# Optimization experiments

Hardware: AMD Instinct MI355X
Metric: run time of the kernel (lower is better)

The kernel has to match this reference:

```python
import jax, jax.numpy as jnp
import numpy as np

WORD_DIM = 200
ASPECT_DIM = 32
NUM_NEG = 2
AVG_RATING = 3.8
LR_RATING = 1.0
LR_ABAE = 1.0


def setup_inputs() -> dict:
    key = jax.random.key(0)
    ks = jax.random.split(key, 20)
    R, L, D, A, B, NNZ = 20000, 30, WORD_DIM, ASPECT_DIM, 4096, 65536
    e_w = jax.random.normal(ks[0], (R, L, D), jnp.float32)
    y_s = jax.random.normal(ks[1], (R, D), jnp.float32)
    z_n = jax.random.normal(ks[2], (R * NUM_NEG, D), jnp.float32)
    label = jax.random.uniform(ks[3], (B,), jnp.float32, 1.0, 5.0)
    u_idx = jnp.stack([jax.random.randint(ks[4], (NNZ,), 0, B),
                       jax.random.randint(ks[5], (NNZ,), 0, R)]).astype(jnp.int64)
    i_idx = jnp.stack([jax.random.randint(ks[6], (NNZ,), 0, B),
                       jax.random.randint(ks[7], (NNZ,), 0, R)]).astype(jnp.int64)
    u_val = jax.random.uniform(ks[8], (NNZ,), jnp.float32)
    i_val = jax.random.uniform(ks[9], (NNZ,), jnp.float32)
    s = 0.05
    M_w = jax.random.normal(ks[10], (D, D), jnp.float32) * s
    M_b = jnp.zeros((D,), jnp.float32)
    W_w = jax.random.normal(ks[11], (A, D), jnp.float32) * s
    W_b = jnp.zeros((A,), jnp.float32)
    T_w = jax.random.normal(ks[12], (D, A), jnp.float32) * s
    T_b = jnp.zeros((D,), jnp.float32)
    fc_w = jax.random.uniform(ks[13], (1, A), jnp.float32, -0.05, 0.05)
    fc_b = jnp.zeros((1,), jnp.float32)
    fm_V = jax.random.uniform(ks[14], (A, 10), jnp.float32, -0.05, 0.05)
    return dict(e_w=e_w, y_s=y_s, z_n=z_n, label=label,
                user_histor_value=u_val, item_histor_value=i_val,
                M_w=M_w, M_b=M_b, W_w=W_w, W_b=W_b, T_w=T_w, T_b=T_b,
                fc_w=fc_w, fc_b=fc_b, fm_V=fm_V,
                user_histor_index=u_idx, item_histor_index=i_idx)


def _l2norm(x, axis):
    return x / jnp.maximum(jnp.linalg.norm(x, axis=axis, keepdims=True), 1e-12)


def reference(e_w, y_s, z_n, label, user_histor_value, item_histor_value,
              M_w, M_b, W_w, W_b, T_w, T_b, fc_w, fc_b, fm_V,
              user_histor_index, item_histor_index):
    R, L, D = e_w.shape
    A = W_w.shape[0]
    B = label.shape[0]
    # ABAE attention: dx = (e_w @ M^T + b) . y_s  -> (R, L)
    Me = jnp.einsum('rld,ed->rle', e_w, M_w) + M_b  # (R, L, D)
    dx = jnp.einsum('rld,rd->rl', Me, y_s)
    ax = jax.nn.softmax(dx, axis=1)                 # attention over words
    z_s = jnp.einsum('rld,rl->rd', e_w, ax)         # (R, D) weighted sentence emb
    p_t = z_s @ W_w.T + W_b                         # (R, A) aspect weights
    r_s = p_t @ T_w.T + T_b                         # (R, D) reconstructed emb
    # margin ranking (hinge) loss on cosine similarities
    c1 = jnp.sum(_l2norm(r_s, 1) * _l2norm(z_s, 1), axis=-1, keepdims=True)  # (R,1)
    c1 = jnp.tile(c1, (1, NUM_NEG)).reshape(-1)                              # (R*neg,)
    zn = _l2norm(z_n.reshape(R, NUM_NEG, D), 2)
    c2 = jnp.sum(zn * _l2norm(r_s, 1)[:, None, :], axis=-1).reshape(-1)
    abae_out_loss = jnp.maximum(0.0, 1.0 - (c1 - c2))
    J_loss = jnp.mean(abae_out_loss)
    # orthogonality regularizer on aspect matrix columns
    Tn = _l2norm(T_w, 0)                            # normalize each column (dim=0)
    G = Tn.T @ Tn                                   # (A, A)
    U_loss = jnp.mean((G - jnp.eye(A, dtype=G.dtype)) ** 2)
    abae_loss = U_loss + J_loss
    # sparse pooling: (B, R) sparse @ (R, A)
    u_rows, u_cols = user_histor_index[0], user_histor_index[1]
    i_rows, i_cols = item_histor_index[0], item_histor_index[1]
    user_aspect = jax.ops.segment_sum(p_t[u_cols] * user_histor_value[:, None],
                                      u_rows, num_segments=B)
    item_aspect = jax.ops.segment_sum(p_t[i_cols] * item_histor_value[:, None],
                                      i_rows, num_segments=B)
    output_emb = user_aspect * item_aspect          # (B, A)
    # factorization machine
    fm_linear = output_emb @ fc_w.T + fc_b          # (B, 1)
    i1 = (output_emb @ fm_V) ** 2
    i2 = (output_emb ** 2) @ (fm_V ** 2)
    # NOTE: faithful to source -- the 0.5*sum reduces over ALL elements (scalar)
    fm_output = 0.5 * jnp.sum(i1 - i2) + fm_linear  # (B, 1)
    prediction = fm_output + jnp.float32(AVG_RATING)
    rating_out_loss = (prediction.reshape(-1) - label) ** 2
    rating_loss = jnp.mean(rating_out_loss)
    obj = LR_RATING * rating_loss + LR_ABAE * abae_loss
    return (obj, rating_out_loss, abae_out_loss, prediction, user_aspect, item_aspect)
```

## Files before the change

kernel.cpp:

```cpp
#include <hip/hip_runtime.h>
#include <hip/hip_bf16.h>
#include <math.h>

#define R_CNT   20000
#define L_CNT   30
#define D_CNT   200
#define A_CNT   32
#define B_CNT   4096
#define NNZ_CNT 65536
#define AVG_RATING 3.8f

#define NW 1536
#define TAIL_GRID 5000

#define OUT_OBJ  0
#define OUT_RL   1
#define OUT_AB   (1 + B_CNT)
#define OUT_PRED (OUT_AB + 2*R_CNT)
#define OUT_UA   (OUT_PRED + B_CNT)
#define OUT_IA   (OUT_UA + B_CNT*A_CNT)

#define WS_DBL    0
#define WS_MODE   32
#define WS_FMLIN  64
#define WS_PT     16448
#define WS_V      2576448
#define WS_JPART  18627648
#define WS_SPART  18667648
#define WS_UPART  18671744

#define WAITV16() do { asm volatile("s_waitcnt vmcnt(16)" ::: "memory"); \
                       __builtin_amdgcn_sched_barrier(0); } while (0)
#define SB0() __builtin_amdgcn_sched_barrier(0)

__device__ __forceinline__ float4 blk_reduce4(float4 v, float4* scratch) {
    __syncthreads();
    #pragma unroll
    for (int o = 32; o >= 1; o >>= 1) {
        v.x += __shfl_xor(v.x, o);
        v.y += __shfl_xor(v.y, o);
        v.z += __shfl_xor(v.z, o);
        v.w += __shfl_xor(v.w, o);
    }
    int w = threadIdx.x >> 6;
    if ((threadIdx.x & 63) == 0) scratch[w] = v;
    __syncthreads();
    float4 t0 = scratch[0], t1 = scratch[1], t2 = scratch[2], t3 = scratch[3];
    return make_float4(t0.x + t1.x + t2.x + t3.x,
                       t0.y + t1.y + t2.y + t3.y,
                       t0.z + t1.z + t2.z + t3.z,
                       t0.w + t1.w + t2.w + t3.w);
}

__global__ __launch_bounds__(256) void k_pre(const float* __restrict__ y_s,
                                             const float* __restrict__ M_w,
                                             const float* __restrict__ T_w,
                                             const int* __restrict__ u_idx,
                                             float* __restrict__ V,
                                             float* __restrict__ upart,
                                             float* __restrict__ out,
                                             double* __restrict__ dbl,
                                             int* __restrict__ mode) {
    __shared__ __align__(16) float sh[8224];
    const int tid = threadIdx.x;
    const int bid = blockIdx.x;

    if (bid < 313) {
        float* Msh = sh;
        float* Ysh = sh + 6500;
        int r0 = bid * 64;
        int dg = tid & 31, rg = tid >> 5;
        float acc[8][8];
        #pragma unroll
        for (int i = 0; i < 8; i++)
            #pragma unroll
            for (int j = 0; j < 8; j++) acc[i][j] = 0.f;
        for (int e0 = 0; e0 < D_CNT; e0 += 25) {
            __syncthreads();
            for (int idx = tid; idx < 25 * 256; idx += 256) {
                int ee = idx >> 8, d = idx & 255;
                Msh[ee * 260 + d] = (d < D_CNT) ? M_w[(e0 + ee) * D_CNT + d] : 0.f;
            }
            for (int idx = tid; idx < 25 * 64; idx += 256) {
                int rr = idx / 25, ee = idx - rr * 25;
                int row = r0 + rr;
                Ysh[ee * 68 + rr] = (row < R_CNT) ? y_s[row * D_CNT + e0 + ee] : 0.f;
            }
            __syncthreads();
            for (int ee = 0; ee < 25; ee++) {
                const float4 ya = *(const float4*)&Ysh[ee * 68 + rg * 8];
                const float4 yb = *(const float4*)&Ysh[ee * 68 + rg * 8 + 4];
                const float4 ma = *(const float4*)&Msh[ee * 260 + dg * 8];
                const float4 mb = *(const float4*)&Msh[ee * 260 + dg * 8 + 4];
                float ys[8] = {ya.x, ya.y, ya.z, ya.w, yb.x, yb.y, yb.z, yb.w};
                float ms[8] = {ma.x, ma.y, ma.z, ma.w, mb.x, mb.y, mb.z, mb.w};
                #pragma unroll
                for (int i = 0; i < 8; i++)
                    #pragma unroll
                    for (int j = 0; j < 8; j++)
                        acc[i][j] = fmaf(ys[i], ms[j], acc[i][j]);
            }
        }
        if (dg < 25) {
            #pragma unroll
            for (int i = 0; i < 8; i++) {
                int row = r0 + rg * 8 + i;
                if (row < R_CNT) {
                    *(float4*)&V[row * D_CNT + dg * 8]     = make_float4(acc[i][0], acc[i][1], acc[i][2], acc[i][3]);
                    *(float4*)&V[row * D_CNT + dg * 8 + 4] = make_float4(acc[i][4], acc[i][5], acc[i][6], acc[i][7]);
                }
            }
        }
    } else if (bid < 345) {
        float* Tsh = sh;
        float* tn  = sh + 6400;
        float4* red4 = (float4*)(sh + 6448);
        for (int idx = tid; idx < 1600; idx += 256)
            ((float4*)Tsh)[idx] = ((const float4*)T_w)[idx];
        __syncthreads();
        int a = tid >> 3, k = tid & 7;
        float p = 0.f;
        #pragma unroll
        for (int j = 0; j < 25; ++j) { float t = Tsh[(k + 8*j)*32 + a]; p = fmaf(t, t, p); }
        p += __shfl_xor(p, 1); p += __shfl_xor(p, 2); p += __shfl_xor(p, 4);
        if (k == 0) tn[a] = fmaxf(sqrtf(p), 1e-12f);
        __syncthreads();
        const int i = bid - 313;
        float s = 0.f;
        #pragma unroll
        for (int j = 0; j < 25; ++j)
            s = fmaf(Tsh[(k + 8*j)*32 + i], Tsh[(k + 8*j)*32 + a], s);
        s += __shfl_xor(s, 1); s += __shfl_xor(s, 2); s += __shfl_xor(s, 4);
        float part = 0.f;
        if (k == 0) {
            float g = s / (tn[i] * tn[a]);
            float diff = g - ((i == a) ? 1.f : 0.f);
            part = diff * diff;
        }
        float4 tot = blk_reduce4(make_float4(part, 0.f, 0.f, 0.f), red4);
        if (tid == 0) upart[i] = tot.x;
    } else {
        int base = (bid - 345) * 2048;
        #pragma unroll
        for (int j = 0; j < 8; ++j)
            out[OUT_UA + base + j * 256 + tid] = 0.f;
        if (bid == 345 && tid == 0) {
            dbl[0] = 0.0; dbl[1] = 0.0; dbl[2] = 0.0;
            int m = 1;
            for (int i = 1; i < 256; i += 2) if (u_idx[i] != 0) { m = 0; break; }
            *mode = m;
        }
    }
}

__device__ __forceinline__ void stage_chunk(const float* src, float* lds,
                                            int lane, const float* ew_last4) {
    #pragma unroll
    for (int i = 0; i < 12; ++i) {
        const float* p = src + i * 256 + lane * 4;
        if (p > ew_last4) p = ew_last4;
        __builtin_amdgcn_global_load_lds(
            (const __attribute__((address_space(1))) unsigned int*)p,
            (__attribute__((address_space(3))) unsigned int*)(lds + i * 256),
            16, 0, 0);
    }
}
__device__ __forceinline__ void stage_v(const float* vsrc, float* lds, int lane) {
    #pragma unroll
    for (int i = 0; i < 4; ++i)
        __builtin_amdgcn_global_load_lds(
            (const __attribute__((address_space(1))) unsigned int*)(vsrc + i * 64 + lane),
            (__attribute__((address_space(3))) unsigned int*)(lds + i * 64),
            4, 0, 0);
}

__device__ __forceinline__ void chunk_pass(const float* __restrict__ eb,
                                           const float* __restrict__ vb,
                                           float* __restrict__ dxs,
                                           int lane, float& m, float& s,
                                           float4& zacc) {
    int l = lane >> 2, k = lane & 3;
    float p = 0.f;
    if (l < 15) {
        const float4* er = (const float4*)(eb + l * 200);
        const float4* vr = (const float4*)vb;
        #pragma unroll
        for (int t = 0; t < 13; ++t) {
            int idx = k + 4 * t;
            if (idx < 50) {
                float4 e = er[idx], v = vr[idx];
                p += e.x * v.x + e.y * v.y + e.z * v.z + e.w * v.w;
            }
        }
    }
    p += __shfl_xor(p, 1);
    p += __shfl_xor(p, 2);
    if (l < 15 && k == 0) dxs[l] = p;
    float4 d0 = ((const float4*)dxs)[0];
    float4 d1 = ((const float4*)dxs)[1];
    float4 d2 = ((const float4*)dxs)[2];
    float4 d3 = ((const float4*)dxs)[3];
    float dx[15] = {d0.x, d0.y, d0.z, d0.w, d1.x, d1.y, d1.z, d1.w,
                    d2.x, d2.y, d2.z, d2.w, d3.x, d3.y, d3.z};
    float cm = dx[0];
    #pragma unroll
    for (int q = 1; q < 15; ++q) cm = fmaxf(cm, dx[q]);
    float mn = fmaxf(m, cm);
    float sc = __expf(m - mn);
    float w[15];
    float ss = 0.f;
    #pragma unroll
    for (int q = 0; q < 15; ++q) { w[q] = __expf(dx[q] - mn); ss += w[q]; }
    s = s * sc + ss;
    zacc.x *= sc; zacc.y *= sc; zacc.z *= sc; zacc.w *= sc;
    if (lane < 50) {
        #pragma unroll
        for (int q = 0; q < 15; ++q) {
            float4 e = ((const float4*)(eb + q * 200))[lane];
            zacc.x = fmaf(w[q], e.x, zacc.x);
            zacc.y = fmaf(w[q], e.y, zacc.y);
            zacc.z = fmaf(w[q], e.z, zacc.z);
            zacc.w = fmaf(w[q], e.w, zacc.w);
        }
    }
    m = mn;
}

__global__ __launch_bounds__(64) void k_zs(const float* __restrict__ e_w,
                                           float* __restrict__ V) {
    __shared__ __align__(16) float bufE[2][3072];
    __shared__ __align__(16) float bufV[2][256];
    const int lane = threadIdx.x;
    const float* ew_last4 = e_w + (size_t)R_CNT * 6000 - 4;

    int rev = blockIdx.x;
    stage_v(V + (size_t)rev * 200, bufV[0], lane);
    stage_chunk(e_w + (size_t)rev * 6000, bufE[0], lane, ew_last4);
    int pv = 0;
    for (;;) {
        float m = -3.0e38f, s = 0.f;
        float4 zacc = make_float4(0.f, 0.f, 0.f, 0.f);
        SB0();
        stage_chunk(e_w + (size_t)rev * 6000 + 3000, bufE[1], lane, ew_last4);
        int rnext = rev + NW;
        bool last = (rnext >= R_CNT);
        int rc = last ? rev : rnext;
        stage_v(V + (size_t)rc * 200, bufV[pv ^ 1], lane);
        WAITV16();
        chunk_pass(bufE[0], bufV[pv], bufV[pv] + 208, lane, m, s, zacc);
        SB0();
        stage_chunk(e_w + (size_t)rc * 6000, bufE[0], lane, ew_last4);
        WAITV16();
        chunk_pass(bufE[1], bufV[pv], bufV[pv] + 208, lane, m, s, zacc);
        float inv = 1.f / s;
        if (lane < 50) {
            float4 z = make_float4(zacc.x * inv, zacc.y * inv,
                                   zacc.z * inv, zacc.w * inv);
            ((float4*)(V + (size_t)rev * 200))[lane] = z;
        }
        if (last) break;
        rev = rnext;
        pv ^= 1;
    }
}

__global__ __launch_bounds__(256) void k_tail(const float* __restrict__ zs,
                                              const float* __restrict__ z_n,
                                              const float* __restrict__ W_w,
                                              const float* __restrict__ W_b,
                                              const float* __restrict__ T_w,
                                              const float* __restrict__ T_b,
                                              float* __restrict__ p_t,
                                              float* __restrict__ out,
                                              double* __restrict__ jpart) {
    __shared__ __align__(16) float zsh[4 * D_CNT];
    __shared__ float pts[4 * 32];
    __shared__ float4 red[8];
    const int tid = threadIdx.x;
    const int w = tid >> 6;
    const int r0 = blockIdx.x * 4;

    for (int i = tid; i < 200; i += 256)
        ((float4*)zsh)[i] = ((const float4*)(zs + (size_t)r0 * D_CNT))[i];

    float zn[8];
    #pragma unroll
    for (int q = 0; q < 8; ++q) zn[q] = 0.f;
    if (tid < D_CNT) {
        #pragma unroll
        for (int q = 0; q < 4; ++q) {
            zn[2*q]   = z_n[(size_t)(2*(r0+q))     * D_CNT + tid];
            zn[2*q+1] = z_n[(size_t)(2*(r0+q) + 1) * D_CNT + tid];
        }
    }
    __syncthreads();

    {
        int a = tid >> 3, k = tid & 7;
        float a0 = 0.f, a1 = 0.f, a2 = 0.f, a3 = 0.f;
        #pragma unroll
        for (int j = 0; j < 25; ++j) {
            float wv = W_w[a * D_CNT + k + 8 * j];
            a0 = fmaf(zsh[0*D_CNT + k + 8*j], wv, a0);
            a1 = fmaf(zsh[1*D_CNT + k + 8*j], wv, a1);
            a2 = fmaf(zsh[2*D_CNT + k + 8*j], wv, a2);
            a3 = fmaf(zsh[3*D_CNT + k + 8*j], wv, a3);
        }
        #pragma unroll
        for (int o = 1; o < 8; o <<= 1) {
            a0 += __shfl_xor(a0, o); a1 += __shfl_xor(a1, o);
            a2 += __shfl_xor(a2, o); a3 += __shfl_xor(a3, o);
        }
        if (k == 0) {
            float wbv = W_b[a];
            float p0 = a0 + wbv, p1 = a1 + wbv, p2 = a2 + wbv, p3 = a3 + wbv;
            pts[0*32+a] = p0; pts[1*32+a] = p1; pts[2*32+a] = p2; pts[3*32+a] = p3;
            p_t[(size_t)(r0+0) * 32 + a] = p0;
            p_t[(size_t)(r0+1) * 32 + a] = p1;
            p_t[(size_t)(r0+2) * 32 + a] = p2;
            p_t[(size_t)(r0+3) * 32 + a] = p3;
        }
    }
    __syncthreads();

    float rv[4] = {0.f, 0.f, 0.f, 0.f};
    float zv[4] = {0.f, 0.f, 0.f, 0.f};
    if (tid < D_CNT) {
        float tbv = T_b[tid];
        rv[0] = tbv; rv[1] = tbv; rv[2] = tbv; rv[3] = tbv;
        const float4* tw = (const float4*)(T_w + tid * 32);
        #pragma unroll
        for (int u = 0; u < 8; ++u) {
            float4 t = tw[u];
            #pragma unroll
            for (int q = 0; q < 4; ++q) {
                rv[q] = fmaf(t.x, pts[q*32 + 4*u + 0], rv[q]);
                rv[q] = fmaf(t.y, pts[q*32 + 4*u + 1], rv[q]);
                rv[q] = fmaf(t.z, pts[q*32 + 4*u + 2], rv[q]);
                rv[q] = fmaf(t.w, pts[q*32 + 4*u + 3], rv[q]);
            }
        }
        #pragma unroll
        for (int q = 0; q < 4; ++q) zv[q] = zsh[q * D_CNT + tid];
    }

    double jloc = 0.0;
    #pragma unroll
    for (int q = 0; q < 4; ++q) {
        float4 Av = make_float4(rv[q]*rv[q], rv[q]*zv[q], zv[q]*zv[q], zn[2*q]*zn[2*q]);
        float4 Bv = make_float4(zn[2*q]*rv[q], zn[2*q+1]*zn[2*q+1], zn[2*q+1]*rv[q], 0.f);
        #pragma unroll
        for (int o = 32; o >= 1; o >>= 1) {
            Av.x += __shfl_xor(Av.x, o); Av.y += __shfl_xor(Av.y, o);
            Av.z += __shfl_xor(Av.z, o); Av.w += __shfl_xor(Av.w, o);
            Bv.x += __shfl_xor(Bv.x, o); Bv.y += __shfl_xor(Bv.y, o);
            Bv.z += __shfl_xor(Bv.z, o);
        }
        if ((tid & 63) == 0) { red[2*w] = Av; red[2*w+1] = Bv; }
        __syncthreads();
        if (tid == 0) {
            float rr = 0.f, rz = 0.f, zz = 0.f, n00 = 0.f, n0r = 0.f, n11 = 0.f, n1r = 0.f;
            #pragma unroll
            for (int i = 0; i < 4; ++i) {
                float4 a = red[2*i], b = red[2*i+1];
                rr += a.x; rz += a.y; zz += a.z; n00 += a.w;
                n0r += b.x; n11 += b.y; n1r += b.z;
            }
            float nr = fmaxf(sqrtf(rr), 1e-12f);
            float nz = fmaxf(sqrtf(zz), 1e-12f);
            float c1  = rz  / (nr * nz);
            float c20 = n0r / (fmaxf(sqrtf(n00), 1e-12f) * nr);
            float c21 = n1r / (fmaxf(sqrtf(n11), 1e-12f) * nr);
            float l0 = fmaxf(0.f, 1.f - (c1 - c20));
            float l1 = fmaxf(0.f, 1.f - (c1 - c21));
            out[OUT_AB + 2 * (r0 + q)]     = l0;
            out[OUT_AB + 2 * (r0 + q) + 1] = l1;
            jloc += (double)l0 + (double)l1;
        }
        __syncthreads();
    }
    if (tid == 0) jpart[blockIdx.x] = jloc;
}

__global__ __launch_bounds__(256) void k_scatter(const int* __restrict__ u_idx,
                                                 const int* __restrict__ i_idx,
                                                 const float* __restrict__ u_val,
                                                 const float* __restrict__ i_val,
                                                 const float* __restrict__ p_t,
                                                 const int* __restrict__ mode,
                                                 float* __restrict__ out) {
    long long gid = (long long)blockIdx.x * 256 + threadIdx.x;
    const long long HALF = (long long)NNZ_CNT * 32;
    int is_item = gid >= HALF;
    long long rem = gid - (is_item ? HALF : 0);
    int k = (int)(rem >> 5), a = (int)(rem & 31);
    const int* idx = is_item ? i_idx : u_idx;
    const float* val = is_item ? i_val : u_val;
    int m64 = *mode;
    int row, col;
    if (m64) { row = idx[2 * k]; col = idx[2 * (NNZ_CNT + k)]; }
    else     { row = idx[k];     col = idx[NNZ_CNT + k]; }
    float v = p_t[col * 32 + a] * val[k];
    float* base = out + (is_item ? OUT_IA : OUT_UA);
    atomicAdd(&base[row * 32 + a], v);
}

__global__ __launch_bounds__(256) void k_fm(const float* __restrict__ out,
                                            const float* __restrict__ fc_w,
                                            const float* __restrict__ fc_b,
                                            const float* __restrict__ fm_V,
                                            float* __restrict__ fm_lin,
                                            double* __restrict__ spart) {
    __shared__ float parts[8];
    int tid = threadIdx.x;
    int a = tid & 31;
    int b = blockIdx.x * 8 + (tid >> 5);
    float ua = out[OUT_UA + b * 32 + a];
    float ia = out[OUT_IA + b * 32 + a];
    float oe = ua * ia;
    float oe2 = oe * oe;
    float lin = oe * fc_w[a];
    #pragma unroll
    for (int o = 1; o < 32; o <<= 1) lin += __shfl_xor(lin, o);
    float part = 0.f;
    #pragma unroll
    for (int j = 0; j < 10; j++) {
        float v = fm_V[a * 10 + j];
        float s1 = oe * v;
        float s2 = oe2 * v * v;
        #pragma unroll
        for (int o = 1; o < 32; o <<= 1) { s1 += __shfl_xor(s1, o); s2 += __shfl_xor(s2, o); }
        part += s1 * s1 - s2;
    }
    if (a == 0) {
        fm_lin[b] = lin + fc_b[0];
        parts[tid >> 5] = part;
    }
    __syncthreads();
    if (tid == 0) {
        float s = 0.f;
        #pragma unroll
        for (int i = 0; i < 8; ++i) s += parts[i];
        spart[blockIdx.x] = 0.5 * (double)s;
    }
}

__global__ __launch_bounds__(256) void k_predfinal(const float* __restrict__ label,
                                                   const float* __restrict__ fm_lin,
                                                   const double* __restrict__ spart,
                                                   const double* __restrict__ jpart,
                                                   const float* __restrict__ upart,
                                                   float* __restrict__ out) {
    __shared__ double dred[4];
    __shared__ float Ssh;
    __shared__ float ured[4];
    int tid = threadIdx.x;
    double sl = spart[tid] + spart[tid + 256];
    #pragma unroll
    for (int o = 32; o >= 1; o >>= 1) sl += __shfl_xor(sl, o);
    if ((tid & 63) == 0) dred[tid >> 6] = sl;
    __syncthreads();
    if (tid == 0) Ssh = (float)(dred[0] + dred[1] + dred[2] + dred[3]);
    __syncthreads();
    float S = Ssh;
    double racc = 0.0;
    #pragma unroll
    for (int i = 0; i < 16; ++i) {
        int b = tid + 256 * i;
        float pred = fm_lin[b] + S + AVG_RATING;
        float d = pred - label[b];
        float rl = d * d;
        out[OUT_PRED + b] = pred;
        out[OUT_RL + b] = rl;
        racc += (double)rl;
    }
    double jacc = 0.0;
    for (int i = tid; i < TAIL_GRID; i += 256) jacc += jpart[i];
    float u = (tid < 32) ? upart[tid] : 0.f;
    #pragma unroll
    for (int o = 32; o >= 1; o >>= 1) {
        racc += __shfl_xor(racc, o);
        jacc += __shfl_xor(jacc, o);
        u    += __shfl_xor(u, o);
    }
    __syncthreads();
    if ((tid & 63) == 0) dred[tid >> 6] = racc;
    __syncthreads();
    double rsum = dred[0] + dred[1] + dred[2] + dred[3];
    __syncthreads();
    if ((tid & 63) == 0) dred[tid >> 6] = jacc;
    __syncthreads();
    double jsum = dred[0] + dred[1] + dred[2] + dred[3];
    if ((tid & 63) == 0) ured[tid >> 6] = u;
    __syncthreads();
    if (tid == 0) {
        double U = (double)(ured[0] + ured[1] + ured[2] + ured[3]) / 1024.0;
        double J = jsum / (2.0 * R_CNT);
        double RL = rsum / (double)B_CNT;
        out[OUT_OBJ] = (float)(RL + U + J);
    }
}

extern "C" void kernel_launch(void* const* d_in, const int* in_sizes, int n_in,
                              void* d_out, int out_size, void* d_ws, size_t ws_size,
                              hipStream_t stream) {
    const float* e_w   = (const float*)d_in[0];
    const float* y_s   = (const float*)d_in[1];
    const float* z_n   = (const float*)d_in[2];
    const float* label = (const float*)d_in[3];
    const float* u_val = (const float*)d_in[4];
    const float* i_val = (const float*)d_in[5];
    const float* M_w   = (const float*)d_in[6];
    const float* W_w   = (const float*)d_in[8];
    const float* W_b   = (const float*)d_in[9];
    const float* T_w   = (const float*)d_in[10];
    const float* T_b   = (const float*)d_in[11];
    const float* fc_w  = (const float*)d_in[12];
    const float* fc_b  = (const float*)d_in[13];
    const float* fm_V  = (const float*)d_in[14];
    const int*   u_idx = (const int*)d_in[15];
    const int*   i_idx = (const int*)d_in[16];

    float* out = (float*)d_out;
    char* ws = (char*)d_ws;
    double* dbl   = (double*)(ws + WS_DBL);
    int* mode     = (int*)(ws + WS_MODE);
    float* fm_lin = (float*)(ws + WS_FMLIN);
    float* p_t    = (float*)(ws + WS_PT);
    float* V      = (float*)(ws + WS_V);
    double* jpart = (double*)(ws + WS_JPART);
    double* spart = (double*)(ws + WS_SPART);
    float* upart  = (float*)(ws + WS_UPART);

    k_pre<<<473, 256, 0, stream>>>(y_s, M_w, T_w, u_idx, V, upart, out, dbl, mode);
    k_zs<<<NW, 64, 0, stream>>>(e_w, V);
    k_tail<<<TAIL_GRID, 256, 0, stream>>>(V, z_n, W_w, W_b, T_w, T_b, p_t, out, jpart);
    k_scatter<<<(2 * NNZ_CNT * 32) / 256, 256, 0, stream>>>(u_idx, i_idx, u_val, i_val,
                                                            p_t, mode, out);
    k_fm<<<B_CNT / 8, 256, 0, stream>>>(out, fc_w, fc_b, fm_V, fm_lin, spart);
    k_predfinal<<<1, 256, 0, stream>>>(label, fm_lin, spart, jpart, upart, out);
}
```

Before: 323.5 us.

## Fuse tail projection and hinge-loss computation into the streaming z_s kernel

Measured after the change: 329.1 us. Within noise of the previous version (+1.7%).

```diff
diff --git a/kernel.cpp b/kernel.cpp
--- a/kernel.cpp
+++ b/kernel.cpp
@@ -11,7 +11,6 @@
 #define AVG_RATING 3.8f
 
 #define NW 1536
-#define TAIL_GRID 5000
 
 #define OUT_OBJ  0
 #define OUT_RL   1
@@ -29,8 +28,8 @@
 #define WS_SPART  18667648
 #define WS_UPART  18671744
 
-#define WAITV16() do { asm volatile("s_waitcnt vmcnt(16)" ::: "memory"); \
-                       __builtin_amdgcn_sched_barrier(0); } while (0)
+#define WAITV(N) do { asm volatile("s_waitcnt vmcnt(" #N ")" ::: "memory"); \
+                      __builtin_amdgcn_sched_barrier(0); } while (0)
 #define SB0() __builtin_amdgcn_sched_barrier(0)
 
 __device__ __forceinline__ float4 blk_reduce4(float4 v, float4* scratch) {
@@ -227,145 +226,121 @@
 }
 
 __global__ __launch_bounds__(64) void k_zs(const float* __restrict__ e_w,
-                                           float* __restrict__ V) {
+                                           const float* __restrict__ V,
+                                           const float* __restrict__ z_n,
+                                           const float* __restrict__ W_w,
+                                           const float* __restrict__ W_b,
+                                           const float* __restrict__ T_w,
+                                           const float* __restrict__ T_b,
+                                           float* __restrict__ p_t,
+                                           float* __restrict__ out,
+                                           double* __restrict__ jpart) {
     __shared__ __align__(16) float bufE[2][3072];
     __shared__ __align__(16) float bufV[2][256];
     const int lane = threadIdx.x;
+    const bool act = lane < 50;
+    const int dl = act ? lane : 0;
     const float* ew_last4 = e_w + (size_t)R_CNT * 6000 - 4;
 
+    const float wb = W_b[lane >> 1];
+    float4 tbv = make_float4(0.f, 0.f, 0.f, 0.f);
+    if (act) tbv = ((const float4*)T_b)[dl];
+    float tb[4] = {tbv.x, tbv.y, tbv.z, tbv.w};
+
+    double jloc = 0.0;
     int rev = blockIdx.x;
     stage_v(V + (size_t)rev * 200, bufV[0], lane);
     stage_chunk(e_w + (size_t)rev * 6000, bufE[0], lane, ew_last4);
     int pv = 0;
     for (;;) {
+        int rnext = rev + NW;
+        bool last = (rnext >= R_CNT);
+        int rc = last ? rev : rnext;
         float m = -3.0e38f, s = 0.f;
         float4 zacc = make_float4(0.f, 0.f, 0.f, 0.f);
         SB0();
         stage_chunk(e_w + (size_t)rev * 6000 + 3000, bufE[1], lane, ew_last4);
-        int rnext = rev + NW;
-        bool last = (rnext >= R_CNT);
-        int rc = last ? rev : rnext;
         stage_v(V + (size_t)rc * 200, bufV[pv ^ 1], lane);
-        WAITV16();
+        float4 zn0 = make_float4(0.f, 0.f, 0.f, 0.f);
+        float4 zn1 = make_float4(0.f, 0.f, 0.f, 0.f);
+        if (act) {
+            zn0 = ((const float4*)(z_n + (size_t)(2 * rev) * 200))[lane];
+            zn1 = ((const float4*)(z_n + (size_t)(2 * rev + 1) * 200))[lane];
+        }
+        WAITV(18);
         chunk_pass(bufE[0], bufV[pv], bufV[pv] + 208, lane, m, s, zacc);
         SB0();
         stage_chunk(e_w + (size_t)rc * 6000, bufE[0], lane, ew_last4);
-        WAITV16();
+        WAITV(18);
         chunk_pass(bufE[1], bufV[pv], bufV[pv] + 208, lane, m, s, zacc);
-        float inv = 1.f / s;
-        if (lane < 50) {
-            float4 z = make_float4(zacc.x * inv, zacc.y * inv,
-                                   zacc.z * inv, zacc.w * inv);
-            ((float4*)(V + (size_t)rev * 200))[lane] = z;
-        }
-        if (last) break;
-        rev = rnext;
-        pv ^= 1;
-    }
-}
-
-__global__ __launch_bounds__(256) void k_tail(const float* __restrict__ zs,
-                                              const float* __restrict__ z_n,
-                                              const float* __restrict__ W_w,
-                                              const float* __restrict__ W_b,
-                                              const float* __restrict__ T_w,
-                                              const float* __restrict__ T_b,
-                                              float* __restrict__ p_t,
-                                              float* __restrict__ out,
-                                              double* __restrict__ jpart) {
-    __shared__ __align__(16) float zsh[4 * D_CNT];
-    __shared__ float pts[4 * 32];
-    __shared__ float4 red[8];
-    const int tid = threadIdx.x;
-    const int w = tid >> 6;
-    const int r0 = blockIdx.x * 4;
-
-    for (int i = tid; i < 200; i += 256)
-        ((float4*)zsh)[i] = ((const float4*)(zs + (size_t)r0 * D_CNT))[i];
-
-    float zn[8];
-    #pragma unroll
-    for (int q = 0; q < 8; ++q) zn[q] = 0.f;
-    if (tid < D_CNT) {
-        #pragma unroll
-        for (int q = 0; q < 4; ++q) {
-            zn[2*q]   = z_n[(size_t)(2*(r0+q))     * D_CNT + tid];
-            zn[2*q+1] = z_n[(size_t)(2*(r0+q) + 1) * D_CNT + tid];
-        }
-    }
-    __syncthreads();
-
-    {
-        int a = tid >> 3, k = tid & 7;
-        float a0 = 0.f, a1 = 0.f, a2 = 0.f, a3 = 0.f;
-        #pragma unroll
-        for (int j = 0; j < 25; ++j) {
-            float wv = W_w[a * D_CNT + k + 8 * j];
-            a0 = fmaf(zsh[0*D_CNT + k + 8*j], wv, a0);
-            a1 = fmaf(zsh[1*D_CNT + k + 8*j], wv, a1);
-            a2 = fmaf(zsh[2*D_CNT + k + 8*j], wv, a2);
-            a3 = fmaf(zsh[3*D_CNT + k + 8*j], wv, a3);
-        }
-        #pragma unroll
-        for (int o = 1; o < 8; o <<= 1) {
-            a0 += __shfl_xor(a0, o); a1 += __shfl_xor(a1, o);
-            a2 += __shfl_xor(a2, o); a3 += __shfl_xor(a3, o);
-        }
-        if (k == 0) {
-            float wbv = W_b[a];
-            float p0 = a0 + wbv, p1 = a1 + wbv, p2 = a2 + wbv, p3 = a3 + wbv;
-            pts[0*32+a] = p0; pts[1*32+a] = p1; pts[2*32+a] = p2; pts[3*32+a] = p3;
-            p_t[(size_t)(r0+0) * 32 + a] = p0;
-            p_t[(size_t)(r0+1) * 32 + a] = p1;
-            p_t[(size_t)(r0+2) * 32 + a] = p2;
-            p_t[(size_t)(r0+3) * 32 + a] = p3;
-        }
-    }
-    __syncthreads();
-
-    float rv[4] = {0.f, 0.f, 0.f, 0.f};
-    float zv[4] = {0.f, 0.f, 0.f, 0.f};
-    if (tid < D_CNT) {
-        float tbv = T_b[tid];
-        rv[0] = tbv; rv[1] = tbv; rv[2] = tbv; rv[3] = tbv;
-        const float4* tw = (const float4*)(T_w + tid * 32);
-        #pragma unroll
-        for (int u = 0; u < 8; ++u) {
-            float4 t = tw[u];
+
+        float* zsh  = bufE[1];
+        float* ptsL = bufE[1] + 208;
+        const float inv = 1.f / s;
+        float zf[4] = {zacc.x * inv, zacc.y * inv, zacc.z * inv, zacc.w * inv};
+        if (act) ((float4*)zsh)[dl] = make_float4(zf[0], zf[1], zf[2], zf[3]);
+
+        {
+            int a = lane >> 1, half = lane & 1;
+            const float4* wrow = (const float4*)(W_w + a * 200);
+            const float4* zrow = (const float4*)zsh;
+            float p = 0.f;
             #pragma unroll
-            for (int q = 0; q < 4; ++q) {
-                rv[q] = fmaf(t.x, pts[q*32 + 4*u + 0], rv[q]);
-                rv[q] = fmaf(t.y, pts[q*32 + 4*u + 1], rv[q]);
-                rv[q] = fmaf(t.z, pts[q*32 + 4*u + 2], rv[q]);
-                rv[q] = fmaf(t.w, pts[q*32 + 4*u + 3], rv[q]);
-            }
-        }
-        #pragma unroll
-        for (int q = 0; q < 4; ++q) zv[q] = zsh[q * D_CNT + tid];
-    }
-
-    double jloc = 0.0;
-    #pragma unroll
-    for (int q = 0; q < 4; ++q) {
-        float4 Av = make_float4(rv[q]*rv[q], rv[q]*zv[q], zv[q]*zv[q], zn[2*q]*zn[2*q]);
-        float4 Bv = make_float4(zn[2*q]*rv[q], zn[2*q+1]*zn[2*q+1], zn[2*q+1]*rv[q], 0.f);
-        #pragma unroll
-        for (int o = 32; o >= 1; o >>= 1) {
-            Av.x += __shfl_xor(Av.x, o); Av.y += __shfl_xor(Av.y, o);
-            Av.z += __shfl_xor(Av.z, o); Av.w += __shfl_xor(Av.w, o);
-            Bv.x += __shfl_xor(Bv.x, o); Bv.y += __shfl_xor(Bv.y, o);
-            Bv.z += __shfl_xor(Bv.z, o);
-        }
-        if ((tid & 63) == 0) { red[2*w] = Av; red[2*w+1] = Bv; }
-        __syncthreads();
-        if (tid == 0) {
-            float rr = 0.f, rz = 0.f, zz = 0.f, n00 = 0.f, n0r = 0.f, n11 = 0.f, n1r = 0.f;
-            #pragma unroll
-            for (int i = 0; i < 4; ++i) {
-                float4 a = red[2*i], b = red[2*i+1];
-                rr += a.x; rz += a.y; zz += a.z; n00 += a.w;
-                n0r += b.x; n11 += b.y; n1r += b.z;
-            }
+            for (int t = 0; t < 25; ++t) {
+                int idx = half + 2 * t;
+                float4 wv = wrow[idx];
+                float4 zv = zrow[idx];
+                p += wv.x * zv.x + wv.y * zv.y + wv.z * zv.z + wv.w * zv.w;
+            }
+            p += __shfl_xor(p, 1);
+            float pt = p + wb;
+            if (half == 0) {
+                ptsL[a] = pt;
+                p_t[(size_t)rev * 32 + a] = pt;
+            }
+        }
+
+        float rr = 0.f, rz = 0.f, zz = 0.f, n00 = 0.f, n0r = 0.f, n11 = 0.f, n1r = 0.f;
+        {
+            const float4* pt4 = (const float4*)ptsL;
+            float4 pq0 = pt4[0], pq1 = pt4[1], pq2 = pt4[2], pq3 = pt4[3];
+            float4 pq4 = pt4[4], pq5 = pt4[5], pq6 = pt4[6], pq7 = pt4[7];
+            if (act) {
+                float znf0[4] = {zn0.x, zn0.y, zn0.z, zn0.w};
+                float znf1[4] = {zn1.x, zn1.y, zn1.z, zn1.w};
+                #pragma unroll
+                for (int j = 0; j < 4; ++j) {
+                    int d = 4 * dl + j;
+                    const float4* trow = (const float4*)(T_w + d * 32);
+                    float r = tb[j];
+                    float4 t0 = trow[0], t1 = trow[1], t2 = trow[2], t3 = trow[3];
+                    float4 t4 = trow[4], t5 = trow[5], t6 = trow[6], t7 = trow[7];
+                    r += t0.x*pq0.x + t0.y*pq0.y + t0.z*pq0.z + t0.w*pq0.w;
+                    r += t1.x*pq1.x + t1.y*pq1.y + t1.z*pq1.z + t1.w*pq1.w;
+                    r += t2.x*pq2.x + t2.y*pq2.y + t2.z*pq2.z + t2.w*pq2.w;
+                    r += t3.x*pq3.x + t3.y*pq3.y + t3.z*pq3.z + t3.w*pq3.w;
+                    r += t4.x*pq4.x + t4.y*pq4.y + t4.z*pq4.z + t4.w*pq4.w;
+                    r += t5.x*pq5.x + t5.y*pq5.y + t5.z*pq5.z + t5.w*pq5.w;
+                    r += t6.x*pq6.x + t6.y*pq6.y + t6.z*pq6.z + t6.w*pq6.w;
+                    r += t7.x*pq7.x + t7.y*pq7.y + t7.z*pq7.z + t7.w*pq7.w;
+                    rr  += r * r;
+                    rz  += r * zf[j];
+                    zz  += zf[j] * zf[j];
+                    n00 += znf0[j] * znf0[j];
+                    n0r += znf0[j] * r;
+                    n11 += znf1[j] * znf1[j];
+                    n1r += znf1[j] * r;
+                }
+            }
+        }
+        #pragma unroll
+        for (int o = 1; o < 64; o <<= 1) {
+            rr  += __shfl_xor(rr, o);  rz  += __shfl_xor(rz, o);
+            zz  += __shfl_xor(zz, o);  n00 += __shfl_xor(n00, o);
+            n0r += __shfl_xor(n0r, o); n11 += __shfl_xor(n11, o);
+            n1r += __shfl_xor(n1r, o);
+        }
+        if (lane == 0) {
             float nr = fmaxf(sqrtf(rr), 1e-12f);
             float nz = fmaxf(sqrtf(zz), 1e-12f);
             float c1  = rz  / (nr * nz);
@@ -373,13 +348,15 @@
             float c21 = n1r / (fmaxf(sqrtf(n11), 1e-12f) * nr);
             float l0 = fmaxf(0.f, 1.f - (c1 - c20));
             float l1 = fmaxf(0.f, 1.f - (c1 - c21));
-            out[OUT_AB + 2 * (r0 + q)]     = l0;
-            out[OUT_AB + 2 * (r0 + q) + 1] = l1;
+            out[OUT_AB + 2 * rev]     = l0;
+            out[OUT_AB + 2 * rev + 1] = l1;
             jloc += (double)l0 + (double)l1;
         }
-        __syncthreads();
-    }
-    if (tid == 0) jpart[blockIdx.x] = jloc;
+        if (last) break;
+        rev = rnext;
+        pv ^= 1;
+    }
+    if (lane == 0) jpart[blockIdx.x] = jloc;
 }
 
 __global__ __launch_bounds__(256) void k_scatter(const int* __restrict__ u_idx,
@@ -475,7 +452,7 @@
         racc += (double)rl;
     }
     double jacc = 0.0;
-    for (int i = tid; i < TAIL_GRID; i += 256) jacc += jpart[i];
+    for (int i = tid; i < NW; i += 256) jacc += jpart[i];
     float u = (tid < 32) ? upart[tid] : 0.f;
     #pragma unroll
     for (int o = 32; o >= 1; o >>= 1) {
@@ -533,8 +510,7 @@
     float* upart  = (float*)(ws + WS_UPART);
 
     k_pre<<<473, 256, 0, stream>>>(y_s, M_w, T_w, u_idx, V, upart, out, dbl, mode);
-    k_zs<<<NW, 64, 0, stream>>>(e_w, V);
-    k_tail<<<TAIL_GRID, 256, 0, stream>>>(V, z_n, W_w, W_b, T_w, T_b, p_t, out, jpart);
+    k_zs<<<NW, 64, 0, stream>>>(e_w, V, z_n, W_w, W_b, T_w, T_b, p_t, out, jpart);
     k_scatter<<<(2 * NNZ_CNT * 32) / 256, 256, 0, stream>>>(u_idx, i_idx, u_val, i_val,
                                                             p_t, mode, out);
     k_fm<<<B_CNT / 8, 256, 0, stream>>>(out, fc_w, fc_b, fm_V, fm_lin, spart);
```
